# Optimization experiments

Measured on AMD Instinct MI355X. Metric: run time of the kernel, lower is better.

## Reference

```python
import jax, jax.numpy as jnp
import numpy as np

NUM_HEADS = 16
HEAD_DIM = 64
INNER = NUM_HEADS * HEAD_DIM  # 1024
QUERY_DIM = 1024
CONTEXT_DIM = 768
SCALE = HEAD_DIM ** -0.5


def setup_inputs() -> dict:
    key = jax.random.key(0)
    ks = jax.random.split(key, 6)
    B, NQ, NKV = 8, 1024, 2048
    query = jax.random.normal(ks[0], (B, NQ, QUERY_DIM), dtype=jnp.float32)
    context = jax.random.normal(ks[1], (B, NKV, CONTEXT_DIM), dtype=jnp.float32)
    # weights stored as [in, out] (transpose of torch Linear), math-equivalent
    w_q = jax.random.normal(ks[2], (QUERY_DIM, INNER), dtype=jnp.float32) * (QUERY_DIM ** -0.5)
    w_kv = jax.random.normal(ks[3], (CONTEXT_DIM, 2 * INNER), dtype=jnp.float32) * (CONTEXT_DIM ** -0.5)
    w_out = jax.random.normal(ks[4], (INNER, QUERY_DIM), dtype=jnp.float32) * (INNER ** -0.5)
    b_out = jax.random.normal(ks[5], (QUERY_DIM,), dtype=jnp.float32) * 0.01
    return {"query": query, "context": context, "w_q": w_q, "w_kv": w_kv,
            "w_out": w_out, "b_out": b_out}


def reference(query, context, w_q, w_kv, w_out, b_out):
    B, NQ, _ = query.shape
    NKV = context.shape[1]
    q = query @ w_q                              # [B, NQ, INNER]
    kv = context @ w_kv                          # [B, NKV, 2*INNER]
    k, v = jnp.split(kv, 2, axis=-1)
    # reshape to [B, H, N, D]
    q = q.reshape(B, NQ, NUM_HEADS, HEAD_DIM).transpose(0, 2, 1, 3)
    k = k.reshape(B, NKV, NUM_HEADS, HEAD_DIM).transpose(0, 2, 1, 3)
    v = v.reshape(B, NKV, NUM_HEADS, HEAD_DIM).transpose(0, 2, 1, 3)
    scores = jnp.einsum('bhqd,bhkd->bhqk', q, k) * SCALE
    attn = jax.nn.softmax(scores, axis=-1)
    out = jnp.einsum('bhqk,bhkd->bhqd', attn, v)  # [B, H, NQ, D]
    out = out.transpose(0, 2, 1, 3).reshape(B, NQ, INNER)
    return out @ w_out + b_out
```

## Files before the change

### kernel.cpp

```cpp
#include <hip/hip_runtime.h>
#include <stdint.h>

typedef __bf16 bf16_t;
typedef bf16_t bf16x8 __attribute__((ext_vector_type(8)));
typedef float f32x4 __attribute__((ext_vector_type(4)));
typedef float f32x16 __attribute__((ext_vector_type(16)));

__device__ __forceinline__ unsigned short f2bf(float x) {
    unsigned u = __builtin_bit_cast(unsigned, x);
    u = (u + 0x7FFFu + ((u >> 16) & 1u)) >> 16;
    return (unsigned short)u;
}

__device__ __forceinline__ unsigned pk_bf16(float lo, float hi) {
    unsigned u0 = __builtin_bit_cast(unsigned, lo) + 0x8000u;
    unsigned u1 = __builtin_bit_cast(unsigned, hi) + 0x8000u;
    return __builtin_amdgcn_perm(u1, u0, 0x07060302u);
}

__device__ __forceinline__ void async_load16(const void* g, void* lds) {
    auto* gp = reinterpret_cast<const __attribute__((address_space(1))) uint32_t*>(
        reinterpret_cast<uintptr_t>(g));
    auto* lp = reinterpret_cast<__attribute__((address_space(3))) uint32_t*>(
        reinterpret_cast<uintptr_t>(lds));
    __builtin_amdgcn_global_load_lds(gp, lp, 16, 0, 0);
}

__global__ __launch_bounds__(256) void cast_f32_bf16(const float* __restrict__ src,
                                                     unsigned short* __restrict__ dst,
                                                     int n8) {
    int i = blockIdx.x * 256 + threadIdx.x;
    if (i >= n8) return;
    const float4* s4 = (const float4*)src;
    float4 a = s4[i * 2], b = s4[i * 2 + 1];
    uint4 o;
    o.x = (unsigned)f2bf(a.x) | ((unsigned)f2bf(a.y) << 16);
    o.y = (unsigned)f2bf(a.z) | ((unsigned)f2bf(a.w) << 16);
    o.z = (unsigned)f2bf(b.x) | ((unsigned)f2bf(b.y) << 16);
    o.w = (unsigned)f2bf(b.z) | ((unsigned)f2bf(b.w) << 16);
    ((uint4*)dst)[i] = o;
}

__global__ __launch_bounds__(256) void transcast(const float* __restrict__ src,
                                                 unsigned short* __restrict__ dst,
                                                 int K, int N, float scale) {
    __shared__ float tile[32][33];
    int x = threadIdx.x, y = threadIdx.y;
    int c0 = blockIdx.x * 32, r0 = blockIdx.y * 32;
    #pragma unroll
    for (int i = 0; i < 32; i += 8)
        tile[y + i][x] = src[(size_t)(r0 + y + i) * N + c0 + x];
    __syncthreads();
    #pragma unroll
    for (int i = 0; i < 32; i += 8)
        dst[(size_t)(c0 + y + i) * K + r0 + x] = f2bf(tile[x][y + i] * scale);
}

template <int EPI>
__global__ __launch_bounds__(256) void gemm_bt(const unsigned short* __restrict__ A,
                                               const unsigned short* __restrict__ Bt,
                                               void* __restrict__ Cout,
                                               const float* __restrict__ bias,
                                               int K, int N, int nkt) {
    __shared__ __align__(16) unsigned short lA[2][128 * 64];
    __shared__ __align__(16) unsigned short lB[2][128 * 64];
    const int tid = threadIdx.x;
    const int w = tid >> 6, l = tid & 63;
    const int wm = w >> 1, wn = w & 1;
    const int row0 = blockIdx.y * 128, col0 = blockIdx.x * 128;
    const int lrow = l & 15, lq = l >> 4;
    const int srow = l >> 3;
    const int scol = ((l & 7) ^ srow) * 8;

    f32x4 acc[4][4];
    #pragma unroll
    for (int i = 0; i < 4; ++i)
        #pragma unroll
        for (int j = 0; j < 4; ++j) acc[i][j] = (f32x4)0.f;

    const unsigned short* ga[4];
    const unsigned short* gb[4];
    #pragma unroll
    for (int q = 0; q < 4; ++q) {
        const int r = (w * 4 + q) * 8 + srow;
        ga[q] = A + (size_t)(row0 + r) * K + scol;
        gb[q] = Bt + (size_t)(col0 + r) * K + scol;
    }

    #pragma unroll
    for (int q = 0; q < 4; ++q) {
        async_load16(ga[q], (char*)lA + (w * 4 + q) * 1024);
        async_load16(gb[q], (char*)lB + (w * 4 + q) * 1024);
        ga[q] += 64;
        gb[q] += 64;
    }
    __syncthreads();

    for (int kt = 0; kt < nkt; ++kt) {
        const int bo = (kt & 1) * 16384;
        if (kt + 1 < nkt) {
            const int bn = bo ^ 16384;
            #pragma unroll
            for (int q = 0; q < 4; ++q) {
                async_load16(ga[q], (char*)lA + bn + (w * 4 + q) * 1024);
                async_load16(gb[q], (char*)lB + bn + (w * 4 + q) * 1024);
                ga[q] += 64;
                gb[q] += 64;
            }
        }
        #pragma unroll
        for (int kc = 0; kc < 2; ++kc) {
            const int pc = ((kc * 4 + lq) ^ (lrow & 7)) * 16;
            bf16x8 af[4], bfr[4];
            #pragma unroll
            for (int i = 0; i < 4; ++i)
                af[i] = *(const bf16x8*)((const char*)lA + bo + (wm * 64 + i * 16 + lrow) * 128 + pc);
            #pragma unroll
            for (int j = 0; j < 4; ++j)
                bfr[j] = *(const bf16x8*)((const char*)lB + bo + (wn * 64 + j * 16 + lrow) * 128 + pc);
            #pragma unroll
            for (int i = 0; i < 4; ++i)
                #pragma unroll
                for (int j = 0; j < 4; ++j)
                    acc[i][j] = __builtin_amdgcn_mfma_f32_16x16x32_bf16(af[i], bfr[j],
                                                                        acc[i][j], 0, 0, 0);
        }
        __syncthreads();
    }
    #pragma unroll
    for (int i = 0; i < 4; ++i) {
        const int grow0 = row0 + wm * 64 + i * 16 + lq * 4;
        #pragma unroll
        for (int j = 0; j < 4; ++j) {
            const int gcol = col0 + wn * 64 + j * 16 + lrow;
            #pragma unroll
            for (int r = 0; r < 4; ++r) {
                float v = acc[i][j][r];
                int grow = grow0 + r;
                if (EPI == 0) {
                    ((unsigned short*)Cout)[(size_t)grow * N + gcol] = f2bf(v);
                } else {
                    ((float*)Cout)[(size_t)grow * N + gcol] = v + bias[gcol];
                }
            }
        }
    }
}

__global__ __launch_bounds__(256, 2) void gemm_kv(const unsigned short* __restrict__ A,
                                                  const unsigned short* __restrict__ Bt,
                                                  unsigned short* __restrict__ Kb,
                                                  unsigned short* __restrict__ Vt) {
    __shared__ __align__(16) unsigned short lA[256 * 64];
    __shared__ __align__(16) unsigned short lB[128 * 64];
    const int tid = threadIdx.x;
    const int w = tid >> 6, l = tid & 63;
    const int wm = w >> 1, wn = w & 1;
    const int row0 = blockIdx.y * 256, col0 = blockIdx.x * 128;
    const int r32 = l & 31, hw = l >> 5;
    const int srow = l >> 3, scol = ((l & 7) ^ srow) * 8;

    f32x16 acc[4][2];
    #pragma unroll
    for (int mi = 0; mi < 4; ++mi)
        #pragma unroll
        for (int ni = 0; ni < 2; ++ni) acc[mi][ni] = (f32x16)0.f;

    const unsigned short* ga = A + (size_t)(row0 + w * 8 + srow) * 768 + scol;
    const unsigned short* gb = Bt + (size_t)(col0 + w * 8 + srow) * 768 + scol;
    char* lAw = (char*)lA + (w * 8) * 128;
    char* lBw = (char*)lB + (w * 8) * 128;
    const char* lap = (const char*)lA + (wm * 128 + r32) * 128;
    const char* lbp = (const char*)lB + (wn * 64 + r32) * 128;
    const int r7 = r32 & 7;

    for (int kt = 0; kt < 12; ++kt) {
        __syncthreads();
        #pragma unroll
        for (int q = 0; q < 8; ++q)
            async_load16(ga + (size_t)q * 32 * 768, lAw + q * 32 * 128);
        #pragma unroll
        for (int q = 0; q < 4; ++q)
            async_load16(gb + (size_t)q * 32 * 768, lBw + q * 32 * 128);
        ga += 64;
        gb += 64;
        __syncthreads();
        #pragma unroll
        for (int ks = 0; ks < 4; ++ks) {
            const int off = ((ks * 2 + hw) ^ r7) * 16;
            bf16x8 af[4], bfr[2];
            #pragma unroll
            for (int mi = 0; mi < 4; ++mi)
                af[mi] = *(const bf16x8*)(lap + mi * 32 * 128 + off);
            #pragma unroll
            for (int ni = 0; ni < 2; ++ni)
                bfr[ni] = *(const bf16x8*)(lbp + ni * 32 * 128 + off);
            #pragma unroll
            for (int mi = 0; mi < 4; ++mi)
                #pragma unroll
                for (int ni = 0; ni < 2; ++ni)
                    acc[mi][ni] = __builtin_amdgcn_mfma_f32_32x32x16_bf16(af[mi], bfr[ni],
                                                                          acc[mi][ni], 0, 0, 0);
        }
    }

    if (col0 < 1024) {
        unsigned short* kp = Kb + (size_t)(row0 + wm * 128) * 1024 + col0 + wn * 64 + r32;
        #pragma unroll
        for (int mi = 0; mi < 4; ++mi)
            #pragma unroll
            for (int ni = 0; ni < 2; ++ni)
                #pragma unroll
                for (int reg = 0; reg < 16; ++reg) {
                    int rr = mi * 32 + (reg & 3) + 8 * (reg >> 2) + 4 * hw;
                    kp[(size_t)rr * 1024 + ni * 32] = f2bf(acc[mi][ni][reg]);
                }
    } else {
        const int bb = row0 >> 11;
        const int keybase = (row0 & 2047) + wm * 128 + 4 * hw;
        const int fvbase = col0 - 1024 + wn * 64 + r32;
        unsigned short* vp = Vt + ((size_t)bb * 1024 + fvbase) * 2048 + keybase;
        #pragma unroll
        for (int mi = 0; mi < 4; ++mi)
            #pragma unroll
            for (int ni = 0; ni < 2; ++ni)
                #pragma unroll
                for (int g = 0; g < 4; ++g) {
                    uint2 pk2;
                    pk2.x = pk_bf16(acc[mi][ni][g * 4 + 0], acc[mi][ni][g * 4 + 1]);
                    pk2.y = pk_bf16(acc[mi][ni][g * 4 + 2], acc[mi][ni][g * 4 + 3]);
                    *(uint2*)(vp + (size_t)(ni * 32) * 2048 + mi * 32 + g * 8) = pk2;
                }
    }
}

__global__ __launch_bounds__(256, 2) void attn_fwd(const unsigned short* __restrict__ qb,
                                                   const unsigned short* __restrict__ kb,
                                                   const unsigned short* __restrict__ vt,
                                                   unsigned short* __restrict__ ob) {
    constexpr int PSTR = 72;
    __shared__ __align__(16) unsigned short lK[2][64 * 64];
    __shared__ __align__(16) unsigned short lV[2][64 * 64];
    __shared__ __align__(16) unsigned short lP[4][32 * PSTR];
    const int tid = threadIdx.x;
    const int w = tid >> 6, l = tid & 63;
    const int bh = blockIdx.x;
    const int b = bh >> 4, h = bh & 15;
    const int q0 = blockIdx.y * 256;
    const int lrow = l & 15, lq = l >> 4;
    const int srow = l >> 3, scol = ((l & 7) ^ (srow & 7)) * 8;

    bf16x8 bq[4][2];
    #pragma unroll
    for (int qs = 0; qs < 4; ++qs)
        #pragma unroll
        for (int kc = 0; kc < 2; ++kc) {
            int row = b * 1024 + q0 + w * 64 + qs * 16 + lrow;
            int col = h * 64 + kc * 32 + lq * 8;
            bq[qs][kc] = *(const bf16x8*)(qb + (size_t)row * 1024 + col);
        }

    f32x4 ot[4][4];
    f32x4 lfr[4];
    #pragma unroll
    for (int qs = 0; qs < 4; ++qs) {
        #pragma unroll
        for (int dt = 0; dt < 4; ++dt) ot[qs][dt] = (f32x4)0.f;
        lfr[qs] = (f32x4)0.f;
    }
    bf16x8 one8;
    #pragma unroll
    for (int i = 0; i < 8; ++i) one8[i] = (bf16_t)1.0f;

    const char* kp0 = (const char*)lK + lrow * 128 + ((lq ^ (lrow & 7)) * 16);
    const char* kp1 = (const char*)lK + lrow * 128 + (((4 + lq) ^ (lrow & 7)) * 16);
    const char* vp0 = (const char*)lV + lrow * 128 + ((lq ^ (lrow & 7)) * 16);
    const char* vp1 = (const char*)lV + lrow * 128 + (((4 + lq) ^ (lrow & 7)) * 16);
    char* pw[2];
    const char* pr[2];
    #pragma unroll
    for (int u = 0; u < 2; ++u) {
        pw[u] = (char*)&lP[w][(u * 16 + lrow) * PSTR + 4 * lq];
        pr[u] = (const char*)&lP[w][(u * 16 + lrow) * PSTR + 8 * lq];
    }

    const unsigned short* gkp = kb + (size_t)b * 2048 * 1024 + h * 64 +
                                (size_t)(w * 8 + srow) * 1024 + scol;
    const unsigned short* gvp = vt + (size_t)(b * 1024 + h * 64) * 2048 +
                                (size_t)(w * 8 + srow) * 2048 + scol;
    char* lKw0 = (char*)lK + (w * 8) * 128;
    char* lKw1 = (char*)lK + (32 + w * 8) * 128;
    char* lVw0 = (char*)lV + (w * 8) * 128;
    char* lVw1 = (char*)lV + (32 + w * 8) * 128;

    async_load16(gkp, lKw0);
    async_load16(gkp + 32 * 1024, lKw1);
    async_load16(gvp, lVw0);
    async_load16(gvp + 32 * 2048, lVw1);
    gkp += 64 * 1024;
    gvp += 64;
    __syncthreads();

    for (int it = 0; it < 32; ++it) {
        const int bo = (it & 1) * 8192;
        if (it < 31) {
            const int bn = bo ^ 8192;
            async_load16(gkp, lKw0 + bn);
            async_load16(gkp + 32 * 1024, lKw1 + bn);
            async_load16(gvp, lVw0 + bn);
            async_load16(gvp + 32 * 2048, lVw1 + bn);
            gkp += 64 * 1024;
            gvp += 64;
        }

        bf16x8 ka[4][2], va[4][2];
        #pragma unroll
        for (int mt = 0; mt < 4; ++mt) {
            ka[mt][0] = *(const bf16x8*)(kp0 + bo + mt * 2048);
            ka[mt][1] = *(const bf16x8*)(kp1 + bo + mt * 2048);
        }
        #pragma unroll
        for (int dt = 0; dt < 4; ++dt) {
            va[dt][0] = *(const bf16x8*)(vp0 + bo + dt * 2048);
            va[dt][1] = *(const bf16x8*)(vp1 + bo + dt * 2048);
        }

        #pragma unroll
        for (int p = 0; p < 2; ++p) {
            f32x4 st[2][4];
            __builtin_amdgcn_s_setprio(1);
            #pragma unroll
            for (int u = 0; u < 2; ++u) {
                const int qs = 2 * p + u;
                #pragma unroll
                for (int mt = 0; mt < 4; ++mt) {
                    f32x4 c = (f32x4)0.f;
                    c = __builtin_amdgcn_mfma_f32_16x16x32_bf16(ka[mt][0], bq[qs][0], c, 0, 0, 0);
                    c = __builtin_amdgcn_mfma_f32_16x16x32_bf16(ka[mt][1], bq[qs][1], c, 0, 0, 0);
                    st[u][mt] = c;
                }
            }
            __builtin_amdgcn_s_setprio(0);
            #pragma unroll
            for (int u = 0; u < 2; ++u) {
                #pragma unroll
                for (int mt = 0; mt < 4; ++mt) {
                    #pragma unroll
                    for (int r = 0; r < 4; ++r)
                        st[u][mt][r] = __builtin_amdgcn_exp2f(st[u][mt][r]);
                    uint2 pk;
                    pk.x = pk_bf16(st[u][mt][0], st[u][mt][1]);
                    pk.y = pk_bf16(st[u][mt][2], st[u][mt][3]);
                    *(uint2*)(pw[u] + 32 * mt) = pk;
                }
            }
            bf16x8 pb[2][2];
            #pragma unroll
            for (int u = 0; u < 2; ++u)
                #pragma unroll
                for (int kcg = 0; kcg < 2; ++kcg)
                    pb[u][kcg] = *(const bf16x8*)(pr[u] + 64 * kcg);
            __builtin_amdgcn_s_setprio(1);
            #pragma unroll
            for (int u = 0; u < 2; ++u) {
                const int qs = 2 * p + u;
                lfr[qs] = __builtin_amdgcn_mfma_f32_16x16x32_bf16(one8, pb[u][0], lfr[qs], 0, 0, 0);
                lfr[qs] = __builtin_amdgcn_mfma_f32_16x16x32_bf16(one8, pb[u][1], lfr[qs], 0, 0, 0);
                #pragma unroll
                for (int dt = 0; dt < 4; ++dt) {
                    ot[qs][dt] = __builtin_amdgcn_mfma_f32_16x16x32_bf16(va[dt][0], pb[u][0], ot[qs][dt], 0, 0, 0);
                    ot[qs][dt] = __builtin_amdgcn_mfma_f32_16x16x32_bf16(va[dt][1], pb[u][1], ot[qs][dt], 0, 0, 0);
                }
            }
            __builtin_amdgcn_s_setprio(0);
        }
        __syncthreads();
    }

    #pragma unroll
    for (int qs = 0; qs < 4; ++qs) {
        float inv = 1.f / lfr[qs][0];
        size_t grow = (size_t)(b * 1024 + q0 + w * 64 + qs * 16 + lrow);
        unsigned short* op = ob + grow * 1024 + h * 64 + 4 * lq;
        #pragma unroll
        for (int dt = 0; dt < 4; ++dt) {
            uint2 pk;
            pk.x = pk_bf16(ot[qs][dt][0] * inv, ot[qs][dt][1] * inv);
            pk.y = pk_bf16(ot[qs][dt][2] * inv, ot[qs][dt][3] * inv);
            *(uint2*)(op + 16 * dt) = pk;
        }
    }
}

extern "C" void kernel_launch(void* const* d_in, const int* in_sizes, int n_in,
                              void* d_out, int out_size, void* d_ws, size_t ws_size,
                              hipStream_t stream) {
    const float* query   = (const float*)d_in[0];
    const float* context = (const float*)d_in[1];
    const float* w_q     = (const float*)d_in[2];
    const float* w_kv    = (const float*)d_in[3];
    const float* w_out   = (const float*)d_in[4];
    const float* b_out   = (const float*)d_in[5];
    float* out = (float*)d_out;

    char* p = (char*)d_ws;
    unsigned short* qin   = (unsigned short*)p; p += (size_t)8192 * 1024 * 2;
    unsigned short* cin   = (unsigned short*)p; p += (size_t)16384 * 768 * 2;
    unsigned short* wqT   = (unsigned short*)p; p += (size_t)1024 * 1024 * 2;
    unsigned short* wkvT  = (unsigned short*)p; p += (size_t)2048 * 768 * 2;
    unsigned short* woutT = (unsigned short*)p; p += (size_t)1024 * 1024 * 2;
    unsigned short* qproj = (unsigned short*)p; p += (size_t)8192 * 1024 * 2;
    unsigned short* kbuf  = (unsigned short*)p; p += (size_t)16384 * 1024 * 2;
    unsigned short* vT    = (unsigned short*)p; p += (size_t)16384 * 1024 * 2;
    unsigned short* obuf  = (unsigned short*)p; p += (size_t)8192 * 1024 * 2;

    const float qscale = 0.125f * 1.44269504088896f;

    cast_f32_bf16<<<8388608 / 8 / 256, 256, 0, stream>>>(query, qin, 8388608 / 8);
    cast_f32_bf16<<<12582912 / 8 / 256, 256, 0, stream>>>(context, cin, 12582912 / 8);
    transcast<<<dim3(32, 32), dim3(32, 8), 0, stream>>>(w_q, wqT, 1024, 1024, qscale);
    transcast<<<dim3(64, 24), dim3(32, 8), 0, stream>>>(w_kv, wkvT, 768, 2048, 1.0f);
    transcast<<<dim3(32, 32), dim3(32, 8), 0, stream>>>(w_out, woutT, 1024, 1024, 1.0f);
    gemm_bt<0><<<dim3(8, 64), 256, 0, stream>>>(qin, wqT, qproj, nullptr, 1024, 1024, 16);
    gemm_kv<<<dim3(16, 64), 256, 0, stream>>>(cin, wkvT, kbuf, vT);
    attn_fwd<<<dim3(128, 4), 256, 0, stream>>>(qproj, kbuf, vT, obuf);
    gemm_bt<2><<<dim3(8, 64), 256, 0, stream>>>(obuf, woutT, out, b_out, 1024, 1024, 16);
}
```

Baseline: 340.4 us.

## Redistribute attention P via permlane swaps instead of LDS, halve query tile

The P-tile round trip through shared memory is replaced with in-register permlane32/permlane16 swaps that move the exp'd score fragments into the B-operand layout. Each block now handles 128 queries instead of 256, which doubles the grid and raises the occupancy target to 4 blocks per CU. The aim is to cut LDS traffic and improve latency hiding. The cost is that each K/V tile loaded into LDS is reused by half as many queries, so global K/V traffic per query doubles.

```diff
diff --git a/kernel.cpp b/kernel.cpp
--- a/kernel.cpp
+++ b/kernel.cpp
@@ -5,6 +5,8 @@
 typedef bf16_t bf16x8 __attribute__((ext_vector_type(8)));
 typedef float f32x4 __attribute__((ext_vector_type(4)));
 typedef float f32x16 __attribute__((ext_vector_type(16)));
+typedef unsigned uint32x2_t __attribute__((ext_vector_type(2)));
+typedef unsigned uint32x4_t __attribute__((ext_vector_type(4)));
 
 __device__ __forceinline__ unsigned short f2bf(float x) {
     unsigned u = __builtin_bit_cast(unsigned, x);
@@ -234,39 +236,37 @@
     }
 }
 
-__global__ __launch_bounds__(256, 2) void attn_fwd(const unsigned short* __restrict__ qb,
+__global__ __launch_bounds__(256, 4) void attn_fwd(const unsigned short* __restrict__ qb,
                                                    const unsigned short* __restrict__ kb,
                                                    const unsigned short* __restrict__ vt,
                                                    unsigned short* __restrict__ ob) {
-    constexpr int PSTR = 72;
     __shared__ __align__(16) unsigned short lK[2][64 * 64];
     __shared__ __align__(16) unsigned short lV[2][64 * 64];
-    __shared__ __align__(16) unsigned short lP[4][32 * PSTR];
     const int tid = threadIdx.x;
     const int w = tid >> 6, l = tid & 63;
     const int bh = blockIdx.x;
     const int b = bh >> 4, h = bh & 15;
-    const int q0 = blockIdx.y * 256;
+    const int q0 = blockIdx.y * 128;
     const int lrow = l & 15, lq = l >> 4;
     const int srow = l >> 3, scol = ((l & 7) ^ (srow & 7)) * 8;
 
-    bf16x8 bq[4][2];
-    #pragma unroll
-    for (int qs = 0; qs < 4; ++qs)
+    bf16x8 bq[2][2];
+    #pragma unroll
+    for (int u = 0; u < 2; ++u)
         #pragma unroll
         for (int kc = 0; kc < 2; ++kc) {
-            int row = b * 1024 + q0 + w * 64 + qs * 16 + lrow;
+            int row = b * 1024 + q0 + w * 32 + u * 16 + lrow;
             int col = h * 64 + kc * 32 + lq * 8;
-            bq[qs][kc] = *(const bf16x8*)(qb + (size_t)row * 1024 + col);
-        }
-
-    f32x4 ot[4][4];
-    f32x4 lfr[4];
-    #pragma unroll
-    for (int qs = 0; qs < 4; ++qs) {
-        #pragma unroll
-        for (int dt = 0; dt < 4; ++dt) ot[qs][dt] = (f32x4)0.f;
-        lfr[qs] = (f32x4)0.f;
+            bq[u][kc] = *(const bf16x8*)(qb + (size_t)row * 1024 + col);
+        }
+
+    f32x4 ot[2][4];
+    f32x4 lfr[2];
+    #pragma unroll
+    for (int u = 0; u < 2; ++u) {
+        #pragma unroll
+        for (int dt = 0; dt < 4; ++dt) ot[u][dt] = (f32x4)0.f;
+        lfr[u] = (f32x4)0.f;
     }
     bf16x8 one8;
     #pragma unroll
@@ -276,13 +276,6 @@
     const char* kp1 = (const char*)lK + lrow * 128 + (((4 + lq) ^ (lrow & 7)) * 16);
     const char* vp0 = (const char*)lV + lrow * 128 + ((lq ^ (lrow & 7)) * 16);
     const char* vp1 = (const char*)lV + lrow * 128 + (((4 + lq) ^ (lrow & 7)) * 16);
-    char* pw[2];
-    const char* pr[2];
-    #pragma unroll
-    for (int u = 0; u < 2; ++u) {
-        pw[u] = (char*)&lP[w][(u * 16 + lrow) * PSTR + 4 * lq];
-        pr[u] = (const char*)&lP[w][(u * 16 + lrow) * PSTR + 8 * lq];
-    }
 
     const unsigned short* gkp = kb + (size_t)b * 2048 * 1024 + h * 64 +
                                 (size_t)(w * 8 + srow) * 1024 + scol;
@@ -313,80 +306,82 @@
             gvp += 64;
         }
 
-        bf16x8 ka[4][2], va[4][2];
+        bf16x8 ka[4][2];
         #pragma unroll
         for (int mt = 0; mt < 4; ++mt) {
             ka[mt][0] = *(const bf16x8*)(kp0 + bo + mt * 2048);
             ka[mt][1] = *(const bf16x8*)(kp1 + bo + mt * 2048);
         }
+
+        unsigned D[2][4][2];
+        __builtin_amdgcn_s_setprio(1);
+        #pragma unroll
+        for (int u = 0; u < 2; ++u) {
+            #pragma unroll
+            for (int mt = 0; mt < 4; ++mt) {
+                f32x4 c = (f32x4)0.f;
+                c = __builtin_amdgcn_mfma_f32_16x16x32_bf16(ka[mt][0], bq[u][0], c, 0, 0, 0);
+                c = __builtin_amdgcn_mfma_f32_16x16x32_bf16(ka[mt][1], bq[u][1], c, 0, 0, 0);
+                #pragma unroll
+                for (int r = 0; r < 4; ++r)
+                    c[r] = __builtin_amdgcn_exp2f(c[r]);
+                D[u][mt][0] = pk_bf16(c[0], c[1]);
+                D[u][mt][1] = pk_bf16(c[2], c[3]);
+            }
+        }
+        __builtin_amdgcn_s_setprio(0);
+
+        bf16x8 pb[2][2];
+        #pragma unroll
+        for (int u = 0; u < 2; ++u) {
+            uint32x4_t pbw[2];
+            #pragma unroll
+            for (int half = 0; half < 2; ++half) {
+                #pragma unroll
+                for (int r2 = 0; r2 < 2; ++r2) {
+                    uint32x2_t t = __builtin_amdgcn_permlane32_swap(
+                        D[u][half * 2][r2], D[u][half * 2 + 1][r2], false, false);
+                    uint32x2_t z = __builtin_amdgcn_permlane16_swap(t.x, t.y, false, false);
+                    pbw[half][r2] = z.x;
+                    pbw[half][r2 + 2] = z.y;
+                }
+            }
+            pb[u][0] = __builtin_bit_cast(bf16x8, pbw[0]);
+            pb[u][1] = __builtin_bit_cast(bf16x8, pbw[1]);
+        }
+
+        bf16x8 va[4][2];
         #pragma unroll
         for (int dt = 0; dt < 4; ++dt) {
             va[dt][0] = *(const bf16x8*)(vp0 + bo + dt * 2048);
             va[dt][1] = *(const bf16x8*)(vp1 + bo + dt * 2048);
         }
 
-        #pragma unroll
-        for (int p = 0; p < 2; ++p) {
-            f32x4 st[2][4];
-            __builtin_amdgcn_s_setprio(1);
-            #pragma unroll
-            for (int u = 0; u < 2; ++u) {
-                const int qs = 2 * p + u;
-                #pragma unroll
-                for (int mt = 0; mt < 4; ++mt) {
-                    f32x4 c = (f32x4)0.f;
-                    c = __builtin_amdgcn_mfma_f32_16x16x32_bf16(ka[mt][0], bq[qs][0], c, 0, 0, 0);
-                    c = __builtin_amdgcn_mfma_f32_16x16x32_bf16(ka[mt][1], bq[qs][1], c, 0, 0, 0);
-                    st[u][mt] = c;
-                }
+        __builtin_amdgcn_s_setprio(1);
+        #pragma unroll
+        for (int u = 0; u < 2; ++u) {
+            lfr[u] = __builtin_amdgcn_mfma_f32_16x16x32_bf16(one8, pb[u][0], lfr[u], 0, 0, 0);
+            lfr[u] = __builtin_amdgcn_mfma_f32_16x16x32_bf16(one8, pb[u][1], lfr[u], 0, 0, 0);
+            #pragma unroll
+            for (int dt = 0; dt < 4; ++dt) {
+                ot[u][dt] = __builtin_amdgcn_mfma_f32_16x16x32_bf16(va[dt][0], pb[u][0], ot[u][dt], 0, 0, 0);
+                ot[u][dt] = __builtin_amdgcn_mfma_f32_16x16x32_bf16(va[dt][1], pb[u][1], ot[u][dt], 0, 0, 0);
             }
-            __builtin_amdgcn_s_setprio(0);
-            #pragma unroll
-            for (int u = 0; u < 2; ++u) {
-                #pragma unroll
-                for (int mt = 0; mt < 4; ++mt) {
-                    #pragma unroll
-                    for (int r = 0; r < 4; ++r)
-                        st[u][mt][r] = __builtin_amdgcn_exp2f(st[u][mt][r]);
-                    uint2 pk;
-                    pk.x = pk_bf16(st[u][mt][0], st[u][mt][1]);
-                    pk.y = pk_bf16(st[u][mt][2], st[u][mt][3]);
-                    *(uint2*)(pw[u] + 32 * mt) = pk;
-                }
-            }
-            bf16x8 pb[2][2];
-            #pragma unroll
-            for (int u = 0; u < 2; ++u)
-                #pragma unroll
-                for (int kcg = 0; kcg < 2; ++kcg)
-                    pb[u][kcg] = *(const bf16x8*)(pr[u] + 64 * kcg);
-            __builtin_amdgcn_s_setprio(1);
-            #pragma unroll
-            for (int u = 0; u < 2; ++u) {
-                const int qs = 2 * p + u;
-                lfr[qs] = __builtin_amdgcn_mfma_f32_16x16x32_bf16(one8, pb[u][0], lfr[qs], 0, 0, 0);
-                lfr[qs] = __builtin_amdgcn_mfma_f32_16x16x32_bf16(one8, pb[u][1], lfr[qs], 0, 0, 0);
-                #pragma unroll
-                for (int dt = 0; dt < 4; ++dt) {
-                    ot[qs][dt] = __builtin_amdgcn_mfma_f32_16x16x32_bf16(va[dt][0], pb[u][0], ot[qs][dt], 0, 0, 0);
-                    ot[qs][dt] = __builtin_amdgcn_mfma_f32_16x16x32_bf16(va[dt][1], pb[u][1], ot[qs][dt], 0, 0, 0);
-                }
-            }
-            __builtin_amdgcn_s_setprio(0);
-        }
+        }
+        __builtin_amdgcn_s_setprio(0);
         __syncthreads();
     }
 
     #pragma unroll
-    for (int qs = 0; qs < 4; ++qs) {
-        float inv = 1.f / lfr[qs][0];
-        size_t grow = (size_t)(b * 1024 + q0 + w * 64 + qs * 16 + lrow);
+    for (int u = 0; u < 2; ++u) {
+        float inv = 1.f / lfr[u][0];
+        size_t grow = (size_t)(b * 1024 + q0 + w * 32 + u * 16 + lrow);
         unsigned short* op = ob + grow * 1024 + h * 64 + 4 * lq;
         #pragma unroll
         for (int dt = 0; dt < 4; ++dt) {
             uint2 pk;
-            pk.x = pk_bf16(ot[qs][dt][0] * inv, ot[qs][dt][1] * inv);
-            pk.y = pk_bf16(ot[qs][dt][2] * inv, ot[qs][dt][3] * inv);
+            pk.x = pk_bf16(ot[u][dt][0] * inv, ot[u][dt][1] * inv);
+            pk.y = pk_bf16(ot[u][dt][2] * inv, ot[u][dt][3] * inv);
             *(uint2*)(op + 16 * dt) = pk;
         }
     }
@@ -423,6 +418,6 @@
     transcast<<<dim3(32, 32), dim3(32, 8), 0, stream>>>(w_out, woutT, 1024, 1024, 1.0f);
     gemm_bt<0><<<dim3(8, 64), 256, 0, stream>>>(qin, wqT, qproj, nullptr, 1024, 1024, 16);
     gemm_kv<<<dim3(16, 64), 256, 0, stream>>>(cin, wkvT, kbuf, vT);
-    attn_fwd<<<dim3(128, 4), 256, 0, stream>>>(qproj, kbuf, vT, obuf);
+    attn_fwd<<<dim3(128, 8), 256, 0, stream>>>(qproj, kbuf, vT, obuf);
     gemm_bt<2><<<dim3(8, 64), 256, 0, stream>>>(obuf, woutT, out, b_out, 1024, 1024, 16);
 }
```

Result: faster. 332.4 us (-2.4%).
